# Performance work log

Hardware: AMD Instinct MI355X
Metric: run time of the kernel (lower is better)

The kernel has to match this reference:

```python
import jax, jax.numpy as jnp
import numpy as np

EMBED_DIM = 1024
NUM_HEADS = 16
HEAD_DIM = EMBED_DIM // NUM_HEADS  # 64
GRID_H, GRID_W = 24, 24
BASE = 10000.0


def rope2d_cache(head_dim=HEAD_DIM, grid_h=GRID_H, grid_w=GRID_W, base=BASE):
    # "Concatenated Embeddings" 2D RoPE cache -> (cos, sin), each [grid_h*grid_w, head_dim]
    pos_dim = head_dim // 2
    inv_freq = 1.0 / (base ** (jnp.arange(0, pos_dim, 2, dtype=jnp.float32) / pos_dim))
    max_grid = max(grid_h, grid_w)
    positions = jnp.arange(max_grid, dtype=jnp.float32)
    freqs = positions[:, None] * inv_freq[None, :]            # [max_grid, pos_dim//2]
    emb_1d = jnp.concatenate([freqs, freqs], axis=-1)          # [max_grid, pos_dim]
    h_emb = jnp.broadcast_to(emb_1d[:grid_h, None, :], (grid_h, grid_w, pos_dim))
    w_emb = jnp.broadcast_to(emb_1d[None, :grid_w, :], (grid_h, grid_w, pos_dim))
    emb_2d = jnp.concatenate([h_emb, w_emb], axis=-1).reshape(-1, head_dim)
    return jnp.cos(emb_2d), jnp.sin(emb_2d)


def rotate_half(x):
    x1, x2 = jnp.split(x, 2, axis=-1)
    return jnp.concatenate([-x2, x1], axis=-1)


def setup_inputs() -> dict:
    key = jax.random.key(0)
    ks = jax.random.split(key, 9)
    B, S, E = 16, GRID_H * GRID_W + 1, EMBED_DIM
    s = 1.0 / np.sqrt(E)
    inp = {
        "hidden_states": jax.random.normal(ks[0], (B, S, E), dtype=jnp.float32),
        "Wq": jax.random.normal(ks[1], (E, E), dtype=jnp.float32) * s,
        "bq": jnp.zeros((E,), dtype=jnp.float32),
        "Wk": jax.random.normal(ks[2], (E, E), dtype=jnp.float32) * s,
        "bk": jnp.zeros((E,), dtype=jnp.float32),
        "Wv": jax.random.normal(ks[3], (E, E), dtype=jnp.float32) * s,
        "bv": jnp.zeros((E,), dtype=jnp.float32),
        "Wo": jax.random.normal(ks[4], (E, E), dtype=jnp.float32) * s,
        "bo": jnp.zeros((E,), dtype=jnp.float32),
    }
    return inp


def reference(hidden_states, Wq, bq, Wk, bk, Wv, bv, Wo, bo):
    B, S, E = hidden_states.shape
    H, D = NUM_HEADS, HEAD_DIM
    scale = D ** -0.5

    def proj(W, b):
        # torch Linear: x @ W.T + b; reshape to [B, H, S, D]
        y = jnp.einsum('bse,fe->bsf', hidden_states, W) + b
        return y.reshape(B, S, H, D).transpose(0, 2, 1, 3)

    q = proj(Wq, bq)
    k = proj(Wk, bk)
    v = proj(Wv, bv)

    cos, sin = rope2d_cache()                 # [num_patches, D]
    cos = cos[None, None, :, :]
    sin = sin[None, None, :, :]

    # CLS token at position 0 is untouched; RoPE applied to patch tokens 1:
    qp = q[:, :, 1:, :]
    kp = k[:, :, 1:, :]
    qp = qp * cos + rotate_half(qp) * sin
    kp = kp * cos + rotate_half(kp) * sin
    q = jnp.concatenate([q[:, :, :1, :], qp], axis=2)
    k = jnp.concatenate([k[:, :, :1, :], kp], axis=2)

    scores = jnp.einsum('bhqd,bhkd->bhqk', q, k) * scale   # [B,H,S,S]
    attn = jax.nn.softmax(scores, axis=-1)
    out = jnp.einsum('bhqk,bhkd->bhqd', attn, v)           # [B,H,S,D]
    out = out.transpose(0, 2, 1, 3).reshape(B, S, E)
    out = jnp.einsum('bse,fe->bsf', out, Wo) + bo
    return out
```

## Files before the change

kernel.cpp:

```cpp
#include <hip/hip_runtime.h>
#include <hip/hip_bf16.h>
#include <stdint.h>

typedef __bf16 bf16_t;
typedef __attribute__((ext_vector_type(4))) float floatx4;
typedef __attribute__((ext_vector_type(8))) __bf16 bf16x8;
typedef __attribute__((ext_vector_type(4))) __bf16 bf16x4;

#define MFMA16(a, b, c) __builtin_amdgcn_mfma_f32_16x16x32_bf16(a, b, c, 0, 0, 0)

#define GLOAD_LDS16(gsrc, ldst)                                                          \
  __builtin_amdgcn_global_load_lds((const __attribute__((address_space(1))) void*)(gsrc),\
                                   (__attribute__((address_space(3))) void*)(ldst),      \
                                   16, 0, 0)

#define BATCH 16
#define SEQ   577
#define EMB   1024
#define NH    16
#define HD    64
#define SPAD  640
#define MROWS (BATCH * SEQ)
#define MPAD  9344

#define EXP_C 0.1803368801111404f

#define OFF_H  0ULL
#define OFF_WQ 19136512ULL
#define OFF_WK 21233664ULL
#define OFF_WV 23330816ULL
#define OFF_WO 25427968ULL
#define OFF_Q  27525120ULL
#define OFF_K  48496640ULL
#define OFF_VT 69468160ULL
#define OFF_AO 90439680ULL

__global__ __launch_bounds__(256) void k_cast(
    const float4* __restrict__ hs, const float4* __restrict__ wq,
    const float4* __restrict__ wk, const float4* __restrict__ wv,
    const float4* __restrict__ wo, bf16x4* __restrict__ hb, bf16x4* __restrict__ wqb,
    bf16x4* __restrict__ wkb, bf16x4* __restrict__ wvb, bf16x4* __restrict__ wob) {
  int idx = blockIdx.x * 256 + threadIdx.x;
  const int H4 = MROWS * EMB / 4;
  const int W4 = EMB * EMB / 4;
  const float4* src;
  bf16x4* dst;
  int i;
  if (idx < H4) {
    src = hs; dst = hb; i = idx;
  } else {
    int r = idx - H4;
    int w = r / W4;
    if (w >= 4) return;
    i = r - w * W4;
    src = (w == 0) ? wq : (w == 1) ? wk : (w == 2) ? wv : wo;
    dst = (w == 0) ? wqb : (w == 1) ? wkb : (w == 2) ? wvb : wob;
  }
  float4 v = src[i];
  bf16x4 o;
  o.x = (bf16_t)v.x; o.y = (bf16_t)v.y; o.z = (bf16_t)v.z; o.w = (bf16_t)v.w;
  dst[i] = o;
}

__global__ __launch_bounds__(256, 3) void k_qkv(const bf16_t* __restrict__ A,
                                                const bf16_t* __restrict__ Wq,
                                                const bf16_t* __restrict__ Wk,
                                                const bf16_t* __restrict__ Wv,
                                                const float* __restrict__ bq,
                                                const float* __restrict__ bk,
                                                const float* __restrict__ bv,
                                                bf16_t* __restrict__ qb,
                                                bf16_t* __restrict__ kb,
                                                bf16_t* __restrict__ vtb) {
  __shared__ __align__(16) bf16_t smem[2 * 10240];
  const int hh = blockIdx.x;
  const int n0 = hh * 64;
  const int m0 = blockIdx.y * 128;
  const int t = threadIdx.x;
  const int wid = t >> 6, lane = t & 63, quad = lane >> 4, c = lane & 15;

  const int srow0 = t >> 2;
  const int srow1 = 64 + srow0;
  const int soff = (((t & 3) ^ ((t >> 3) & 3)) * 8);

#define QKV_STAGE(buf, k0)                                                                  \
  {                                                                                         \
    bf16_t* As_ = smem + (buf) * 10240;                                                     \
    bf16_t* Bs_ = As_ + 4096;                                                               \
    GLOAD_LDS16(A + (size_t)(m0 + srow0) * EMB + (k0) + soff, (char*)As_ + (wid * 64) * 16);\
    GLOAD_LDS16(A + (size_t)(m0 + srow1) * EMB + (k0) + soff,                               \
                (char*)As_ + (256 + wid * 64) * 16);                                        \
    GLOAD_LDS16(Wq + (size_t)(n0 + srow0) * EMB + (k0) + soff, (char*)Bs_ + (wid * 64) * 16);\
    GLOAD_LDS16(Wk + (size_t)(n0 + srow0) * EMB + (k0) + soff,                              \
                (char*)Bs_ + 4096 + (wid * 64) * 16);                                       \
    GLOAD_LDS16(Wv + (size_t)(n0 + srow0) * EMB + (k0) + soff,                              \
                (char*)Bs_ + 8192 + (wid * 64) * 16);                                       \
  }

  floatx4 acc[3][2][4];
#pragma unroll
  for (int z = 0; z < 3; z++)
#pragma unroll
    for (int i = 0; i < 2; i++)
#pragma unroll
      for (int j = 0; j < 4; j++) {
        floatx4 zz = {0.f, 0.f, 0.f, 0.f};
        acc[z][i][j] = zz;
      }

  QKV_STAGE(0, 0);
  __syncthreads();
  int cur = 0;
  for (int kt = 0; kt < 32; kt++) {
    if (kt < 31) QKV_STAGE(cur ^ 1, (kt + 1) * 32);
    const bf16_t* Asc = smem + cur * 10240;
    const bf16_t* Bsc = Asc + 4096;
    bf16x8 af[2];
#pragma unroll
    for (int mi = 0; mi < 2; mi++) {
      int row = wid * 32 + mi * 16 + c;
      af[mi] = *(const bf16x8*)(Asc + row * 32 + (quad * 8 ^ (((row >> 1) & 3) << 3)));
    }
#pragma unroll
    for (int z = 0; z < 3; z++) {
      bf16x8 bfr[4];
#pragma unroll
      for (int ni = 0; ni < 4; ni++) {
        int row = ni * 16 + c;
        bfr[ni] = *(const bf16x8*)(Bsc + z * 2048 + row * 32 + (quad * 8 ^ (((row >> 1) & 3) << 3)));
      }
#pragma unroll
      for (int mi = 0; mi < 2; mi++)
#pragma unroll
        for (int ni = 0; ni < 4; ni++) acc[z][mi][ni] = MFMA16(af[mi], bfr[ni], acc[z][mi][ni]);
    }
    __syncthreads();
    cur ^= 1;
  }
#undef QKV_STAGE

  const float invf = exp2f(-(float)c * 0.8304820237218405f);

  for (int z = 0; z < 3; z++) {
    const float* bias = (z == 0) ? bq : (z == 1) ? bk : bv;
    float bias_v[4];
#pragma unroll
    for (int ni = 0; ni < 4; ni++) bias_v[ni] = bias[n0 + ni * 16 + c];
#pragma unroll
    for (int mi = 0; mi < 2; mi++) {
#pragma unroll
      for (int r = 0; r < 4; r++) {
        int m = m0 + wid * 32 + mi * 16 + quad * 4 + r;
        if (m >= MROWS) continue;
        int bb = m / SEQ;
        int s = m - bb * SEQ;
        if (z < 2) {
          float ch = 1.f, sh = 0.f, cw = 1.f, sw = 0.f;
          if (s > 0) {
            int p = s - 1;
            int hp = p / 24, wp2 = p - (p / 24) * 24;
            __sincosf((float)hp * invf, &sh, &ch);
            __sincosf((float)wp2 * invf, &sw, &cw);
          }
          bf16_t* dst = (z == 0) ? qb : kb;
          size_t rowoff = ((size_t)(bb * NH + hh) * SPAD + s) * HD;
#pragma unroll
          for (int ni = 0; ni < 4; ni++) {
            float val = acc[z][mi][ni][r] + bias_v[ni];
            float part = acc[z][mi][ni ^ 2][r] + bias_v[ni ^ 2];
            float rot = (ni < 2) ? -part : part;
            float cs = (ni < 2) ? ch : cw;
            float sn = (ni < 2) ? sh : sw;
            dst[rowoff + ni * 16 + c] = (bf16_t)(val * cs + rot * sn);
          }
        } else {
          size_t base = (size_t)(bb * NH + hh) * HD;
#pragma unroll
          for (int ni = 0; ni < 4; ni++) {
            float val = acc[z][mi][ni][r] + bias_v[ni];
            int d = ni * 16 + c;
            vtb[(base + d) * SPAD + s] = (bf16_t)val;
          }
        }
      }
    }
  }
}

#define PSTR 72
#define OSTR 66
__global__ __launch_bounds__(256, 4) void k_attn(const bf16_t* __restrict__ qb,
                                                 const bf16_t* __restrict__ kb,
                                                 const bf16_t* __restrict__ vtb,
                                                 bf16_t* __restrict__ ao) {
  __shared__ __align__(16) bf16_t smem[13824];
  bf16_t* Ks = smem;
  bf16_t* Vs = smem + 4608;
  bf16_t* Ps = smem + 9216;
  const int t = threadIdx.x, wid = t >> 6, lane = t & 63, quad = lane >> 4, c = lane & 15;
  const int hh = blockIdx.x, bb = blockIdx.y, qt = blockIdx.z;
  const size_t bh = (size_t)bb * NH + hh;
  const bf16_t* qbase = qb + bh * SPAD * HD + (size_t)qt * 128 * HD;
  const bf16_t* kbase = kb + bh * SPAD * HD;
  const bf16_t* vbase = vtb + bh * HD * SPAD;
  bf16_t* Pw = Ps + wid * 1152;

  bf16x8 aq[2][2];
#pragma unroll
  for (int mi = 0; mi < 2; mi++)
#pragma unroll
    for (int h = 0; h < 2; h++)
      aq[mi][h] = *(const bf16x8*)(qbase + (size_t)(wid * 32 + mi * 16 + c) * HD + h * 32 + quad * 8);

  uint4 kr[2], vr[2];
#pragma unroll
  for (int j = 0; j < 2; j++) {
    int ci = j * 256 + t;
    int row = ci >> 3, off = (ci & 7) * 8;
    kr[j] = *(const uint4*)(kbase + (size_t)row * HD + off);
    vr[j] = *(const uint4*)(vbase + (size_t)row * SPAD + off);
  }

  floatx4 acc_o[2][4];
  float lsum[2][4];
#pragma unroll
  for (int mi = 0; mi < 2; mi++) {
    floatx4 z = {0.f, 0.f, 0.f, 0.f};
#pragma unroll
    for (int nd = 0; nd < 4; nd++) acc_o[mi][nd] = z;
#pragma unroll
    for (int r = 0; r < 4; r++) lsum[mi][r] = 0.f;
  }

  for (int kt = 0; kt < 9; kt++) {
    __syncthreads();
#pragma unroll
    for (int j = 0; j < 2; j++) {
      int ci = j * 256 + t;
      int row = ci >> 3, off = (ci & 7) * 8;
      *(uint4*)((char*)Ks + (row * PSTR + off) * 2) = kr[j];
      *(uint4*)((char*)Vs + (row * PSTR + off) * 2) = vr[j];
    }
    __syncthreads();
    if (kt < 8) {
#pragma unroll
      for (int j = 0; j < 2; j++) {
        int ci = j * 256 + t;
        int row = ci >> 3, off = (ci & 7) * 8;
        kr[j] = *(const uint4*)(kbase + (size_t)((kt + 1) * 64 + row) * HD + off);
        vr[j] = *(const uint4*)(vbase + (size_t)row * SPAD + (kt + 1) * 64 + off);
      }
    }

    floatx4 sc[2][4];
#pragma unroll
    for (int ni = 0; ni < 4; ni++) {
      bf16x8 k0 = *(const bf16x8*)(Ks + (ni * 16 + c) * PSTR + quad * 8);
      bf16x8 k1 = *(const bf16x8*)(Ks + (ni * 16 + c) * PSTR + 32 + quad * 8);
#pragma unroll
      for (int mi = 0; mi < 2; mi++) {
        floatx4 zz = {0.f, 0.f, 0.f, 0.f};
        zz = MFMA16(aq[mi][0], k0, zz);
        zz = MFMA16(aq[mi][1], k1, zz);
        sc[mi][ni] = zz;
      }
    }

#pragma unroll
    for (int mi = 0; mi < 2; mi++) {
#pragma unroll
      for (int ni = 0; ni < 4; ni++)
#pragma unroll
        for (int r = 0; r < 4; r++) {
          float p = exp2f(sc[mi][ni][r] * EXP_C);
          lsum[mi][r] += p;
          Pw[(quad * 4 + r) * PSTR + ni * 16 + c] = (bf16_t)p;
        }
      bf16x8 pa0 = *(const bf16x8*)(Pw + c * PSTR + quad * 8);
      bf16x8 pa1 = *(const bf16x8*)(Pw + c * PSTR + 32 + quad * 8);
#pragma unroll
      for (int nd = 0; nd < 4; nd++) {
        bf16x8 v0 = *(const bf16x8*)(Vs + (nd * 16 + c) * PSTR + quad * 8);
        bf16x8 v1 = *(const bf16x8*)(Vs + (nd * 16 + c) * PSTR + 32 + quad * 8);
        acc_o[mi][nd] = MFMA16(pa0, v0, acc_o[mi][nd]);
        acc_o[mi][nd] = MFMA16(pa1, v1, acc_o[mi][nd]);
      }
    }
  }

  {
    bf16x8 klast[2];
#pragma unroll
    for (int h = 0; h < 2; h++) {
      bf16x8 kk;
#pragma unroll
      for (int i = 0; i < 8; i++) kk[i] = (bf16_t)0.0f;
      if (c == 0) kk = *(const bf16x8*)(kbase + (size_t)576 * HD + h * 32 + quad * 8);
      klast[h] = kk;
    }
    float vlast[4];
#pragma unroll
    for (int nd = 0; nd < 4; nd++)
      vlast[nd] = (float)vbase[(size_t)(nd * 16 + c) * SPAD + 576];
#pragma unroll
    for (int mi = 0; mi < 2; mi++) {
      floatx4 zz = {0.f, 0.f, 0.f, 0.f};
      zz = MFMA16(aq[mi][0], klast[0], zz);
      zz = MFMA16(aq[mi][1], klast[1], zz);
#pragma unroll
      for (int r = 0; r < 4; r++) {
        float p = exp2f(zz[r] * EXP_C);
        p = __shfl(p, quad * 16, 64);
#pragma unroll
        for (int nd = 0; nd < 4; nd++) acc_o[mi][nd][r] += p * vlast[nd];
        if (c == 0) lsum[mi][r] += p;
      }
    }
  }

#pragma unroll
  for (int mi = 0; mi < 2; mi++)
#pragma unroll
    for (int r = 0; r < 4; r++) {
      float l = lsum[mi][r];
      l += __shfl_xor(l, 1, 64);
      l += __shfl_xor(l, 2, 64);
      l += __shfl_xor(l, 4, 64);
      l += __shfl_xor(l, 8, 64);
      lsum[mi][r] = l;
    }

  {
    const int rsub = lane >> 3, c8 = lane & 7;
#pragma unroll
    for (int mi = 0; mi < 2; mi++) {
#pragma unroll
      for (int r = 0; r < 4; r++) {
        float inv_l = 1.f / lsum[mi][r];
        int row = quad * 4 + r;
#pragma unroll
        for (int nd = 0; nd < 4; nd++)
          Pw[row * OSTR + nd * 16 + c] = (bf16_t)(acc_o[mi][nd][r] * inv_l);
      }
#pragma unroll
      for (int j = 0; j < 2; j++) {
        int row = j * 8 + rsub;
        bf16x8 ov = *(const bf16x8*)(Pw + row * OSTR + c8 * 8);
        int q = qt * 128 + wid * 32 + mi * 16 + row;
        if (q < SEQ) {
          size_t mrow = (size_t)bb * SEQ + q;
          *(bf16x8*)(ao + mrow * EMB + hh * HD + c8 * 8) = ov;
        }
      }
    }
  }
}

__global__ __launch_bounds__(256) void k_oproj(const bf16_t* __restrict__ A,
                                               const bf16_t* __restrict__ Wo,
                                               const float* __restrict__ bo,
                                               float* __restrict__ out) {
  __shared__ __align__(16) bf16_t smem[2 * 8192];
  const int n0 = blockIdx.x * 128, m0 = blockIdx.y * 128;
  const int t = threadIdx.x;
  const int wid = t >> 6, lane = t & 63, quad = lane >> 4, c = lane & 15;
  const int wr = wid >> 1, wc = wid & 1;
  const int srow0 = t >> 2;
  const int srow1 = 64 + srow0;
  const int soff = (((t & 3) ^ ((t >> 3) & 3)) * 8);

#define OPROJ_STAGE(buf, k0)                                                                 \
  {                                                                                          \
    bf16_t* As_ = smem + (buf) * 8192;                                                       \
    bf16_t* Bs_ = As_ + 4096;                                                                \
    GLOAD_LDS16(A + (size_t)(m0 + srow0) * EMB + (k0) + soff, (char*)As_ + (wid * 64) * 16); \
    GLOAD_LDS16(A + (size_t)(m0 + srow1) * EMB + (k0) + soff,                                \
                (char*)As_ + (256 + wid * 64) * 16);                                         \
    GLOAD_LDS16(Wo + (size_t)(n0 + srow0) * EMB + (k0) + soff, (char*)Bs_ + (wid * 64) * 16);\
    GLOAD_LDS16(Wo + (size_t)(n0 + srow1) * EMB + (k0) + soff,                               \
                (char*)Bs_ + (256 + wid * 64) * 16);                                         \
  }

  floatx4 acc[4][4];
#pragma unroll
  for (int i = 0; i < 4; i++)
#pragma unroll
    for (int j = 0; j < 4; j++) {
      floatx4 z = {0.f, 0.f, 0.f, 0.f};
      acc[i][j] = z;
    }

  OPROJ_STAGE(0, 0);
  __syncthreads();
  int cur = 0;
  for (int kt = 0; kt < 32; kt++) {
    if (kt < 31) OPROJ_STAGE(cur ^ 1, (kt + 1) * 32);
    const bf16_t* Asc = smem + cur * 8192;
    const bf16_t* Bsc = Asc + 4096;
    bf16x8 af[4], bfr[4];
#pragma unroll
    for (int mi = 0; mi < 4; mi++) {
      int row = wr * 64 + mi * 16 + c;
      af[mi] = *(const bf16x8*)(Asc + row * 32 + (quad * 8 ^ (((row >> 1) & 3) << 3)));
    }
#pragma unroll
    for (int ni = 0; ni < 4; ni++) {
      int row = wc * 64 + ni * 16 + c;
      bfr[ni] = *(const bf16x8*)(Bsc + row * 32 + (quad * 8 ^ (((row >> 1) & 3) << 3)));
    }
#pragma unroll
    for (int mi = 0; mi < 4; mi++)
#pragma unroll
      for (int ni = 0; ni < 4; ni++) acc[mi][ni] = MFMA16(af[mi], bfr[ni], acc[mi][ni]);
    __syncthreads();
    cur ^= 1;
  }
#undef OPROJ_STAGE

  float bias_v[4];
#pragma unroll
  for (int ni = 0; ni < 4; ni++) bias_v[ni] = bo[n0 + wc * 64 + ni * 16 + c];
#pragma unroll
  for (int mi = 0; mi < 4; mi++)
#pragma unroll
    for (int r = 0; r < 4; r++) {
      int m = m0 + wr * 64 + mi * 16 + quad * 4 + r;
      if (m >= MROWS) continue;
#pragma unroll
      for (int ni = 0; ni < 4; ni++)
        out[(size_t)m * EMB + n0 + wc * 64 + ni * 16 + c] = acc[mi][ni][r] + bias_v[ni];
    }
}

extern "C" void kernel_launch(void* const* d_in, const int* in_sizes, int n_in, void* d_out,
                              int out_size, void* d_ws, size_t ws_size, hipStream_t stream) {
  const float* hs = (const float*)d_in[0];
  const float* Wq = (const float*)d_in[1];
  const float* bq = (const float*)d_in[2];
  const float* Wk = (const float*)d_in[3];
  const float* bk = (const float*)d_in[4];
  const float* Wv = (const float*)d_in[5];
  const float* bv = (const float*)d_in[6];
  const float* Wo = (const float*)d_in[7];
  const float* bo = (const float*)d_in[8];
  float* out = (float*)d_out;
  char* ws = (char*)d_ws;

  bf16_t* hb = (bf16_t*)(ws + OFF_H);
  bf16_t* wqb = (bf16_t*)(ws + OFF_WQ);
  bf16_t* wkb = (bf16_t*)(ws + OFF_WK);
  bf16_t* wvb = (bf16_t*)(ws + OFF_WV);
  bf16_t* wob = (bf16_t*)(ws + OFF_WO);
  bf16_t* qbuf = (bf16_t*)(ws + OFF_Q);
  bf16_t* kbuf = (bf16_t*)(ws + OFF_K);
  bf16_t* vtbuf = (bf16_t*)(ws + OFF_VT);
  bf16_t* aob = (bf16_t*)(ws + OFF_AO);


  k_cast<<<13328, 256, 0, stream>>>((const float4*)hs, (const float4*)Wq, (const float4*)Wk,
                                    (const float4*)Wv, (const float4*)Wo, (bf16x4*)hb,
                                    (bf16x4*)wqb, (bf16x4*)wkb, (bf16x4*)wvb, (bf16x4*)wob);

  dim3 gq(16, 73);
  k_qkv<<<gq, 256, 0, stream>>>(hb, wqb, wkb, wvb, bq, bk, bv, qbuf, kbuf, vtbuf);

  dim3 ga(16, 16, 5);
  k_attn<<<ga, 256, 0, stream>>>(qbuf, kbuf, vtbuf, aob);

  dim3 go(8, 73);
  k_oproj<<<go, 256, 0, stream>>>(aob, wob, bo, out);
}
```

Before: 323.8 us.

## Enlarge attention query tile to 192 rows and handle last query row separately

Each attention block now processes 192 query rows (three 16-row MFMA tiles per wave instead of two), so the grid drops from 5 to 3 query tiles per head. K/V tiles staged in LDS are reused across more queries, and less padded work is done. The one leftover query row (index 576) is computed by the last block with a scalar dot-product/softmax/PV pass through LDS. In exchange, register pressure rises (launch bounds lowered to 3 blocks/SM), there are fewer blocks overall, and the tail pass is serial work on one block.

Measured after the change: 312.8 us. 3.4% less time.

```diff
diff --git a/kernel.cpp b/kernel.cpp
--- a/kernel.cpp
+++ b/kernel.cpp
@@ -189,7 +189,8 @@
 
 #define PSTR 72
 #define OSTR 66
-__global__ __launch_bounds__(256, 4) void k_attn(const bf16_t* __restrict__ qb,
+#define MI   3
+__global__ __launch_bounds__(256, 3) void k_attn(const bf16_t* __restrict__ qb,
                                                  const bf16_t* __restrict__ kb,
                                                  const bf16_t* __restrict__ vtb,
                                                  bf16_t* __restrict__ ao) {
@@ -200,17 +201,18 @@
   const int t = threadIdx.x, wid = t >> 6, lane = t & 63, quad = lane >> 4, c = lane & 15;
   const int hh = blockIdx.x, bb = blockIdx.y, qt = blockIdx.z;
   const size_t bh = (size_t)bb * NH + hh;
-  const bf16_t* qbase = qb + bh * SPAD * HD + (size_t)qt * 128 * HD;
+  const bf16_t* qall = qb + bh * SPAD * HD;
+  const bf16_t* qbase = qall + (size_t)qt * 192 * HD;
   const bf16_t* kbase = kb + bh * SPAD * HD;
   const bf16_t* vbase = vtb + bh * HD * SPAD;
   bf16_t* Pw = Ps + wid * 1152;
 
-  bf16x8 aq[2][2];
-#pragma unroll
-  for (int mi = 0; mi < 2; mi++)
+  bf16x8 aq[MI][2];
+#pragma unroll
+  for (int mi = 0; mi < MI; mi++)
 #pragma unroll
     for (int h = 0; h < 2; h++)
-      aq[mi][h] = *(const bf16x8*)(qbase + (size_t)(wid * 32 + mi * 16 + c) * HD + h * 32 + quad * 8);
+      aq[mi][h] = *(const bf16x8*)(qbase + (size_t)(wid * 48 + mi * 16 + c) * HD + h * 32 + quad * 8);
 
   uint4 kr[2], vr[2];
 #pragma unroll
@@ -221,10 +223,10 @@
     vr[j] = *(const uint4*)(vbase + (size_t)row * SPAD + off);
   }
 
-  floatx4 acc_o[2][4];
-  float lsum[2][4];
-#pragma unroll
-  for (int mi = 0; mi < 2; mi++) {
+  floatx4 acc_o[MI][4];
+  float lsum[MI][4];
+#pragma unroll
+  for (int mi = 0; mi < MI; mi++) {
     floatx4 z = {0.f, 0.f, 0.f, 0.f};
 #pragma unroll
     for (int nd = 0; nd < 4; nd++) acc_o[mi][nd] = z;
@@ -252,13 +254,13 @@
       }
     }
 
-    floatx4 sc[2][4];
+    floatx4 sc[MI][4];
 #pragma unroll
     for (int ni = 0; ni < 4; ni++) {
       bf16x8 k0 = *(const bf16x8*)(Ks + (ni * 16 + c) * PSTR + quad * 8);
       bf16x8 k1 = *(const bf16x8*)(Ks + (ni * 16 + c) * PSTR + 32 + quad * 8);
 #pragma unroll
-      for (int mi = 0; mi < 2; mi++) {
+      for (int mi = 0; mi < MI; mi++) {
         floatx4 zz = {0.f, 0.f, 0.f, 0.f};
         zz = MFMA16(aq[mi][0], k0, zz);
         zz = MFMA16(aq[mi][1], k1, zz);
@@ -267,7 +269,7 @@
     }
 
 #pragma unroll
-    for (int mi = 0; mi < 2; mi++) {
+    for (int mi = 0; mi < MI; mi++) {
 #pragma unroll
       for (int ni = 0; ni < 4; ni++)
 #pragma unroll
@@ -303,7 +305,7 @@
     for (int nd = 0; nd < 4; nd++)
       vlast[nd] = (float)vbase[(size_t)(nd * 16 + c) * SPAD + 576];
 #pragma unroll
-    for (int mi = 0; mi < 2; mi++) {
+    for (int mi = 0; mi < MI; mi++) {
       floatx4 zz = {0.f, 0.f, 0.f, 0.f};
       zz = MFMA16(aq[mi][0], klast[0], zz);
       zz = MFMA16(aq[mi][1], klast[1], zz);
@@ -319,7 +321,7 @@
   }
 
 #pragma unroll
-  for (int mi = 0; mi < 2; mi++)
+  for (int mi = 0; mi < MI; mi++)
 #pragma unroll
     for (int r = 0; r < 4; r++) {
       float l = lsum[mi][r];
@@ -333,7 +335,7 @@
   {
     const int rsub = lane >> 3, c8 = lane & 7;
 #pragma unroll
-    for (int mi = 0; mi < 2; mi++) {
+    for (int mi = 0; mi < MI; mi++) {
 #pragma unroll
       for (int r = 0; r < 4; r++) {
         float inv_l = 1.f / lsum[mi][r];
@@ -346,12 +348,55 @@
       for (int j = 0; j < 2; j++) {
         int row = j * 8 + rsub;
         bf16x8 ov = *(const bf16x8*)(Pw + row * OSTR + c8 * 8);
-        int q = qt * 128 + wid * 32 + mi * 16 + row;
+        int q = qt * 192 + wid * 48 + mi * 16 + row;
         if (q < SEQ) {
           size_t mrow = (size_t)bb * SEQ + q;
           *(bf16x8*)(ao + mrow * EMB + hh * HD + c8 * 8) = ov;
         }
       }
+    }
+  }
+
+  if (qt == 2) {
+    float* Pt = (float*)Ks;
+    float* Ot = Pt + 584;
+    __syncthreads();
+    bf16x8 qv8[8];
+    const bf16_t* q576 = qall + (size_t)576 * HD;
+#pragma unroll
+    for (int ch = 0; ch < 8; ch++) qv8[ch] = *(const bf16x8*)(q576 + ch * 8);
+#pragma unroll
+    for (int rep = 0; rep < 3; rep++) {
+      int j = t + rep * 256;
+      if (j < SEQ) {
+        const bf16_t* krow = kbase + (size_t)j * HD;
+        float s = 0.f;
+#pragma unroll
+        for (int ch = 0; ch < 8; ch++) {
+          bf16x8 kx = *(const bf16x8*)(krow + ch * 8);
+#pragma unroll
+          for (int e = 0; e < 8; e++) s += (float)qv8[ch][e] * (float)kx[e];
+        }
+        Pt[j] = exp2f(s * EXP_C);
+      }
+    }
+    __syncthreads();
+    {
+      int d = t & 63, g = t >> 6;
+      int j0 = g * 145, j1 = (g == 3) ? SEQ : (j0 + 145);
+      const bf16_t* vrow = vbase + (size_t)d * SPAD;
+      float o = 0.f;
+      for (int j = j0; j < j1; j++) o += Pt[j] * (float)vrow[j];
+      Ot[g * 64 + d] = o;
+    }
+    __syncthreads();
+    if (wid == 0) {
+      float l = 0.f;
+      for (int k2 = lane; k2 < SEQ; k2 += 64) l += Pt[k2];
+#pragma unroll
+      for (int off = 1; off < 64; off <<= 1) l += __shfl_xor(l, off, 64);
+      float sum = Ot[lane] + Ot[64 + lane] + Ot[128 + lane] + Ot[192 + lane];
+      ao[((size_t)bb * SEQ + 576) * EMB + hh * HD + lane] = (bf16_t)(sum / l);
     }
   }
 }
@@ -464,7 +509,7 @@
   dim3 gq(16, 73);
   k_qkv<<<gq, 256, 0, stream>>>(hb, wqb, wkb, wvb, bq, bk, bv, qbuf, kbuf, vtbuf);
 
-  dim3 ga(16, 16, 5);
+  dim3 ga(16, 16, 3);
   k_attn<<<ga, 256, 0, stream>>>(qbuf, kbuf, vtbuf, aob);
 
   dim3 go(8, 73);
```
